# Optimization experiments

Hardware: AMD Instinct MI355X
Metric: run time of the kernel (lower is better)

## Reference

```python
import jax, jax.numpy as jnp
import numpy as np

# ---- static config (mirrors PaCoVoxelLoss init) ----
NUM_QUERIES = 20
FACTOR = 64
NUM_GT = 12
K_NEIGHBORS = 8          # repulsion.num_neighbors
REP_EPS = 1e-12          # repulsion.epsilon
BANDWIDTH = 0.03         # repulsion.kernel_bandwidth
RADIUS = 0.07            # repulsion.radius
ALPHA_PARAM = 0.5
BETA_CHAMFER = 20.0
W_CLS, W_REP, W_CH1, W_CH2 = 1.0, 1.0, 1.0, 1.0
PAD_COST = 1e6           # pad value to square the rectangular assignment problem


def _hungarian(cost):
    # Jonker-Volgenant / e-maxx shortest augmenting path; cost: (n, n) float64.
    # Returns col_to_row: for each column j, the row assigned to it.
    n = cost.shape[0]
    INF = 1e18
    u = np.zeros(n + 1); v = np.zeros(n + 1)
    p = np.zeros(n + 1, dtype=np.int64)
    way = np.zeros(n + 1, dtype=np.int64)
    for i in range(1, n + 1):
        p[0] = i; j0 = 0
        minv = np.full(n + 1, INF)
        used = np.zeros(n + 1, dtype=bool)
        while True:
            used[j0] = True
            i0 = p[j0]; delta = INF; j1 = 0
            for j in range(1, n + 1):
                if not used[j]:
                    cur = cost[i0 - 1, j - 1] - u[i0] - v[j]
                    if cur < minv[j]:
                        minv[j] = cur; way[j] = j0
                    if minv[j] < delta:
                        delta = minv[j]; j1 = j
            for j in range(n + 1):
                if used[j]:
                    u[p[j]] += delta; v[j] -= delta
                else:
                    minv[j] -= delta
            j0 = j1
            if p[j0] == 0:
                break
        while j0 != 0:
            j1 = way[j0]; p[j0] = p[j1]; j0 = j1
    return p[1:] - 1


def _match(cost_np):
    # cost_np: (B, Q, P) with P <= Q -> rows (B, P): pred row matched to each gt col.
    Bn, Qn, Pn = cost_np.shape
    rows = np.zeros((Bn, Pn), dtype=np.int64)
    for b in range(Bn):
        sq = np.full((Qn, Qn), PAD_COST, dtype=np.float64)
        sq[:, :Pn] = cost_np[b].astype(np.float64)
        rows[b] = _hungarian(sq)[:Pn]
    return rows


def _gather_q(A, rows):
    # A: (B, Q, P), rows: (B, P) -> A[b, rows[b,p], p] : (B, P)
    return jnp.take_along_axis(A, rows[:, None, :], axis=1)[:, 0, :]


def _bce_logits(x, t):
    return jnp.maximum(x, 0.0) - x * t + jnp.log1p(jnp.exp(-jnp.abs(x)))


def _cost_terms(pred_normals, pred_distances, gt_normals, gt_distances, points, gt_masks):
    mask_f = gt_masks.astype(points.dtype)           # (B, P, N)
    cnt = mask_f.sum(-1)                             # (B, P)
    # |points . n_q - d_q| for all query planes: (B, Q, N)
    pp = jnp.abs(jnp.einsum('bnd,bqd->bqn', points, pred_normals) - pred_distances[:, :, None])
    cham_raw = jnp.einsum('bqn,bpn->bqp', pp, mask_f) / jnp.maximum(cnt, 1.0)[:, None, :]
    has = (cnt > 0)[:, None, :]                      # (B, 1, P)
    normal_sim = 1.0 - jnp.abs(jnp.einsum('bqd,bpd->bqp', pred_normals, gt_normals))
    dist_diff = jnp.abs(pred_distances[:, :, None] - gt_distances[:, None, :])
    cost = normal_sim + 0.5 * dist_diff + 5.0 * jnp.where(has, cham_raw, 1.0)
    return cost, cham_raw, normal_sim, dist_diff, has


def _losses(pred_logits, pred_normals, pred_distances, gt_normals, gt_distances,
            points, reconstructed_points, gt, gt_masks, rows):
    _, cham_raw, normal_sim, dist_diff, has = _cost_terms(
        pred_normals, pred_distances, gt_normals, gt_distances, points, gt_masks)

    # classification loss: target 1 at matched pred rows
    Qn = pred_logits.shape[1]
    cls_target = jax.nn.one_hot(rows, Qn, dtype=pred_logits.dtype).sum(axis=1)  # (B, Q)
    cls_loss = _bce_logits(pred_logits, cls_target).mean()

    # param loss over matched pairs (mean over P matches, mean over B)
    param_loss = (_gather_q(normal_sim, rows).mean(-1) + _gather_q(dist_diff, rows).mean(-1)).mean()

    # pvd chamfer: point-to-plane term, zero for empty masks, /P /B
    pvd_chamfer = _gather_q(jnp.where(has, cham_raw, 0.0), rows).mean()

    # repulsion loss on per-query point groups
    Bn = reconstructed_points.shape[0]
    rp = reconstructed_points.reshape(Bn, NUM_QUERIES, FACTOR, 3)
    d2 = jnp.sum((rp[:, :, :, None, :] - rp[:, :, None, :, :]) ** 2, axis=-1)  # (B,Q,F,F)
    _, idx = jax.lax.top_k(-d2, K_NEIGHBORS)       # k nearest incl. self
    dn = jnp.maximum(jnp.take_along_axis(d2, idx[..., 1:], axis=-1), REP_EPS)  # (B,Q,F,k-1)
    w = jnp.exp(-dn / BANDWIDTH ** 2)
    rep = jnp.maximum(jnp.mean((RADIUS - jnp.sqrt(dn)) * w, axis=(2, 3)), 0.0).mean()

    # fine-grained chamfer (L1 and L2) between reconstructed and gt clouds
    diff = reconstructed_points[:, :, None, :] - gt[:, None, :, :]  # (B, M, G, 3)
    d1 = jnp.abs(diff).sum(-1)
    d2c = (diff ** 2).sum(-1)
    ch1 = (0.5 * (d1.min(axis=2).mean(axis=1) + d1.min(axis=1).mean(axis=1))).mean()
    ch2 = (0.5 * (d2c.min(axis=2).mean(axis=1) + d2c.min(axis=1).mean(axis=1))).mean()

    total = (W_CLS * cls_loss + ALPHA_PARAM * param_loss + BETA_CHAMFER * pvd_chamfer
             + W_REP * rep + W_CH1 * ch1 + W_CH2 * ch2)
    return total


def setup_inputs() -> dict:
    key = jax.random.key(0)
    ks = jax.random.split(key, 10)
    B, Q, P, N, G = 8, NUM_QUERIES, NUM_GT, 4096, 2048

    def unit(k, shape):
        v = jax.random.normal(k, shape, dtype=jnp.float32)
        return v / jnp.linalg.norm(v, axis=-1, keepdims=True)

    return {
        'pred_logits': jax.random.normal(ks[0], (B, Q), dtype=jnp.float32),
        'pred_normals': unit(ks[1], (B, Q, 3)),
        'pred_distances': jax.random.normal(ks[2], (B, Q), dtype=jnp.float32),
        'gt_normals': unit(ks[3], (B, P, 3)),
        'gt_distances': jax.random.normal(ks[4], (B, P), dtype=jnp.float32),
        'gt_masks': jax.random.bernoulli(ks[5], 0.3, (B, P, N)),
        'points': jax.random.normal(ks[6], (B, N, 3), dtype=jnp.float32),
        'reconstructed_points': 0.5 * jax.random.normal(ks[7], (B, Q * FACTOR, 3), dtype=jnp.float32),
        'gt': jax.random.normal(ks[8], (B, G, 3), dtype=jnp.float32),
        'gt_index': jax.random.randint(ks[9], (B, G), 0, P, dtype=jnp.int64) if jax.config.jax_enable_x64 else jax.random.randint(ks[9], (B, G), 0, P, dtype=jnp.int32),
    }


def reference(pred_logits, pred_normals, pred_distances, gt_normals, gt_distances,
              points, reconstructed_points, gt, gt_masks, gt_index):
    cost = _cost_terms(pred_normals, pred_distances, gt_normals, gt_distances, points, gt_masks)[0]
    rows = jnp.asarray(_match(np.asarray(cost)))  # Hungarian (host, like scipy in original)
    return _losses(pred_logits, pred_normals, pred_distances, gt_normals, gt_distances,
                   points, reconstructed_points, gt, gt_masks, rows)
```

## Files before the change

kernel.cpp:

```cpp
#include <hip/hip_runtime.h>
#include <math.h>

#define Bn 8
#define Qn 20
#define Pn 12
#define Nn 4096
#define Gn 2048
#define Mn 1280
#define Fn 64
#define KNB 7
#define NCOST 160
#define NREP 40
#define NBLK 616
#define C2_TARGET 616
#define SCOPE_AGENT __HIP_MEMORY_SCOPE_AGENT


__device__ __forceinline__ float aread(float* p) { return atomicAdd(p, 0.0f); }
__device__ __forceinline__ void ast(float* p, float v) {
    __hip_atomic_store(p, v, __ATOMIC_RELAXED, SCOPE_AGENT);
}
__device__ __forceinline__ float ald(const float* p) {
    return __hip_atomic_load(p, __ATOMIC_RELAXED, SCOPE_AGENT);
}

__device__ __forceinline__ int rdlane_i(int v, int l) {
    return __builtin_amdgcn_readlane(v, l);
}
__device__ __forceinline__ float rdlane_f(float v, int l) {
    return __int_as_float(__builtin_amdgcn_readlane(__float_as_int(v), l));
}
__device__ __forceinline__ unsigned wave_min_u32(unsigned x) {
    unsigned t;
    t = (unsigned)__builtin_amdgcn_update_dpp((int)0xFFFFFFFF, (int)x, 0x111, 0xF, 0xF, false);
    x = t < x ? t : x;
    t = (unsigned)__builtin_amdgcn_update_dpp((int)0xFFFFFFFF, (int)x, 0x112, 0xF, 0xF, false);
    x = t < x ? t : x;
    t = (unsigned)__builtin_amdgcn_update_dpp((int)0xFFFFFFFF, (int)x, 0x114, 0xF, 0xF, false);
    x = t < x ? t : x;
    t = (unsigned)__builtin_amdgcn_update_dpp((int)0xFFFFFFFF, (int)x, 0x118, 0xF, 0xF, false);
    x = t < x ? t : x;
    t = (unsigned)__builtin_amdgcn_update_dpp((int)0xFFFFFFFF, (int)x, 0x142, 0xF, 0xF, false);
    x = t < x ? t : x;
    t = (unsigned)__builtin_amdgcn_update_dpp((int)0xFFFFFFFF, (int)x, 0x143, 0xF, 0xF, false);
    x = t < x ? t : x;
    return x;
}

__device__ __forceinline__ void wait_zero(float* ws, unsigned init) {
    unsigned* z = (unsigned*)(ws + 7785);
    while (__hip_atomic_load(z, __ATOMIC_ACQUIRE, SCOPE_AGENT) - init != 1u)
        __builtin_amdgcn_s_sleep(1);
}

__device__ __forceinline__ void bump_c2(float* ws, float* out, unsigned init) {
    unsigned* c2P = (unsigned*)(ws + 7784);
    unsigned old = __hip_atomic_fetch_add(c2P, 1u, __ATOMIC_ACQ_REL, SCOPE_AGENT);
    if (old - init == (unsigned)(C2_TARGET - 1)) {
        float* acc = ws + 7776;
        float a0 = aread(&acc[0]);
        float a1 = aread(&acc[1]);
        float a2 = aread(&acc[2]);
        float a3 = aread(&acc[3]);
        float a4 = aread(&acc[4]);
        float a5 = aread(&acc[5]);
        out[0] = a0 + 0.5f * a1 + 20.f * a2 + a3 + a4 + a5;
        unsigned* w = (unsigned*)ws;
        __hip_atomic_store(&w[7782], init, __ATOMIC_RELAXED, SCOPE_AGENT);
        __hip_atomic_store(&w[7784], init, __ATOMIC_RELAXED, SCOPE_AGENT);
        __hip_atomic_store(&w[7785], init, __ATOMIC_RELAXED, SCOPE_AGENT);
        __hip_atomic_store(&w[7786], init, __ATOMIC_RELAXED, SCOPE_AGENT);
        for (int k = 0; k < 40; ++k)
            __hip_atomic_store(&w[8040 + k], init, __ATOMIC_RELAXED, SCOPE_AGENT);
        for (int k = 0; k < 64; ++k)
            __hip_atomic_store(&w[8080 + k], init, __ATOMIC_RELAXED, SCOPE_AGENT);
    }
}

__global__ void fused_kernel(const float* __restrict__ pred_logits,
                             const float* __restrict__ pred_normals,
                             const float* __restrict__ pred_distances,
                             const float* __restrict__ gt_normals,
                             const float* __restrict__ gt_distances,
                             const float* __restrict__ points,
                             const int*   __restrict__ gt_masks,
                             const float* __restrict__ recon,
                             const float* __restrict__ gt,
                             float* __restrict__ ws,
                             float* __restrict__ out) {
    __shared__ __align__(16) float smem[2 * Pn * 256];
    __shared__ int sflag;
    const int blk = blockIdx.x;
    const int tid = threadIdx.x;

    float* cham = ws;
    float* ns   = ws + 1920;
    float* dd   = ws + 3840;
    float* cost = ws + 5760;
    float* cnt  = ws + 7680;
    float* acc  = ws + 7776;
    unsigned* doneP = (unsigned*)(ws + 7782);
    unsigned* baseP = (unsigned*)(ws + 7783);
    unsigned* repcP = (unsigned*)(ws + 7786);
    unsigned* chunkA = (unsigned*)(ws + 8040);
    unsigned* chunkB = (unsigned*)(ws + 8080);
    float* rep_part = ws + 7808;
    float* pmA1 = ws + 8192;
    float* pmA2 = ws + 90112;
    float* pmB1 = ws + 172032;
    float* pmB2 = ws + 253952;

    const unsigned init = __hip_atomic_load(baseP, __ATOMIC_RELAXED, SCOPE_AGENT);

    if (blk < NCOST) {
        if (blk == 0 && tid < 6) ast(&acc[tid], 0.f);
        const int b = blk / Qn, q = blk % Qn;
        const float nx = pred_normals[(b * Qn + q) * 3 + 0];
        const float ny = pred_normals[(b * Qn + q) * 3 + 1];
        const float nz = pred_normals[(b * Qn + q) * 3 + 2];
        const float dq = pred_distances[b * Qn + q];

        float accs[Pn], accw[Pn];
#pragma unroll
        for (int p = 0; p < Pn; ++p) { accs[p] = 0.f; accw[p] = 0.f; }

        const float* ptb = points + (size_t)b * Nn * 3;
        const int*   mb  = gt_masks + (size_t)b * Pn * Nn;

        for (int n = tid; n < Nn; n += 256) {
            float px = ptb[n * 3 + 0], py = ptb[n * 3 + 1], pz = ptb[n * 3 + 2];
            float pp = fabsf(px * nx + py * ny + pz * nz - dq);
#pragma unroll
            for (int p = 0; p < Pn; ++p) {
                float m = (float)mb[(size_t)p * Nn + n];
                accs[p] += pp * m;
                accw[p] += m;
            }
        }
#pragma unroll
        for (int p = 0; p < Pn; ++p) {
            smem[p * 256 + tid] = accs[p];
            smem[(p + Pn) * 256 + tid] = accw[p];
        }
        __syncthreads();
        for (int off = 128; off > 0; off >>= 1) {
            if (tid < off) {
#pragma unroll
                for (int r = 0; r < 2 * Pn; ++r) smem[r * 256 + tid] += smem[r * 256 + tid + off];
            }
            __syncthreads();
        }
        if (tid < Pn) {
            const int p = tid;
            float c  = smem[(p + Pn) * 256];
            float cv = smem[p * 256] / fmaxf(c, 1.f);
            float gnx = gt_normals[(b * Pn + p) * 3 + 0];
            float gny = gt_normals[(b * Pn + p) * 3 + 1];
            float gnz = gt_normals[(b * Pn + p) * 3 + 2];
            float nsim = 1.f - fabsf(nx * gnx + ny * gny + nz * gnz);
            float ddv  = fabsf(dq - gt_distances[b * Pn + p]);
            int idx = (b * Qn + q) * Pn + p;
            ast(&cham[idx], cv);
            ast(&ns[idx],   nsim);
            ast(&dd[idx],   ddv);
            ast(&cost[idx], nsim + 0.5f * ddv + 5.f * ((c > 0.f) ? cv : 1.f));
            if (q == 0) ast(&cnt[b * Pn + p], c);
        }
        __syncthreads();
        if (tid == 0) {
            if (blk == 0) {
                unsigned* z = (unsigned*)(ws + 7785);
                __hip_atomic_store(z, init + 1u, __ATOMIC_RELEASE, SCOPE_AGENT);
            }
            __hip_atomic_fetch_add(doneP, 1u, __ATOMIC_RELEASE, SCOPE_AGENT);
        }

        if (blk >= 8) {
            if (tid == 0) bump_c2(ws, out, init);
            return;
        }

        if (tid == 0) {
            while (__hip_atomic_load(doneP, __ATOMIC_RELAXED, SCOPE_AGENT) - init != (unsigned)NCOST)
                __builtin_amdgcn_s_sleep(2);
            (void)__hip_atomic_load(doneP, __ATOMIC_ACQUIRE, SCOPE_AGENT);
        }
        __syncthreads();

        if (tid < 64) {
            const int b2 = blk;
            const int t = tid;
            const int col = t;
            const bool isCol = (col >= 1 && col <= Qn);

            float cr[Pn];
#pragma unroll
            for (int k = 0; k < Pn; ++k) cr[k] = 0.f;
            if (isCol) {
                const float* cb = cost + ((size_t)b2 * Qn + (col - 1)) * Pn;
#pragma unroll
                for (int k = 0; k < Pn; ++k) cr[k] = ald(&cb[k]);
            }

            float v = 0.f, u = 0.f, minv = 0.f;
            int way = 0, p = 0;

            for (int i = 1; i <= Pn; ++i) {
                minv = 1e30f;
                bool used = false;
                bool rowInPath = false;
                int j0s = 0;
                while (true) {
                    if (col == j0s) used = true;
                    int i0s = (j0s == 0) ? i : rdlane_i(p, j0s);
                    if (t == i0s) rowInPath = true;
                    float u_i0 = rdlane_f(u, i0s);
                    const int bs = i0s - 1;
                    float l10 = (bs & 1) ? cr[1]  : cr[0];
                    float l11 = (bs & 1) ? cr[3]  : cr[2];
                    float l12 = (bs & 1) ? cr[5]  : cr[4];
                    float l13 = (bs & 1) ? cr[7]  : cr[6];
                    float l14 = (bs & 1) ? cr[9]  : cr[8];
                    float l15 = (bs & 1) ? cr[11] : cr[10];
                    float l20 = (bs & 2) ? l11 : l10;
                    float l21 = (bs & 2) ? l13 : l12;
                    float l22 = (bs & 2) ? l15 : l14;
                    float cij = (bs >= 8) ? l22 : ((bs >= 4) ? l21 : l20);
                    if (isCol && !used) {
                        float cur = cij - u_i0 - v;
                        if (cur < minv) { minv = cur; way = j0s; }
                    }
                    float mv = (isCol && !used) ? minv : 1e30f;
                    unsigned kb = __float_as_uint(mv);
                    kb = ((int)kb < 0) ? ~kb : (kb | 0x80000000u);
                    kb = (kb & ~31u) | (unsigned)(col & 31);
                    unsigned kmin = (unsigned)rdlane_i((int)wave_min_u32(kb), 63);
                    int j1 = (int)(kmin & 31u);
                    float delta = rdlane_f(minv, j1);
                    if (used || col == 0) v -= delta;
                    else if (isCol)       minv -= delta;
                    if (rowInPath)        u += delta;
                    j0s = j1;
                    int pj0 = rdlane_i(p, j0s);
                    if (pj0 == 0) break;
                }
                while (j0s != 0) {
                    int wj = rdlane_i(way, j0s);
                    int pw = (wj == 0) ? i : rdlane_i(p, wj);
                    if (col == j0s) p = pw;
                    j0s = wj;
                }
            }

            float cls = 0.f, par = 0.f, pvd = 0.f;
            if (isCol) {
                float x = pred_logits[b2 * Qn + (col - 1)];
                float tgt = (p > 0) ? 1.f : 0.f;
                cls = fmaxf(x, 0.f) - x * tgt + log1pf(expf(-fabsf(x)));
                if (p > 0) {
                    int idx = (b2 * Qn + (col - 1)) * Pn + (p - 1);
                    par = ald(&ns[idx]) + ald(&dd[idx]);
                    pvd = (ald(&cnt[b2 * Pn + (p - 1)]) > 0.f) ? ald(&cham[idx]) : 0.f;
                }
            }
            for (int off = 32; off > 0; off >>= 1) {
                cls += __shfl_down(cls, off);
                par += __shfl_down(par, off);
                pvd += __shfl_down(pvd, off);
            }
            if (t == 0) {
                atomicAdd(&acc[0], cls / (float)(Bn * Qn));
                atomicAdd(&acc[1], par / (float)(Bn * Pn));
                atomicAdd(&acc[2], pvd / (float)(Bn * Pn));
                bump_c2(ws, out, init);
            }
        }
        return;
    } else if (blk < 200) {
        const int wave = tid >> 6, lane = tid & 63;
        const int g = (blk - NCOST) * 4 + wave;
        float* xs = smem + wave * 192;
        float* ys = xs + 64;
        float* zs = xs + 128;
        const float* base = recon + (size_t)g * Fn * 3;
        xs[lane] = base[lane * 3 + 0];
        ys[lane] = base[lane * 3 + 1];
        zs[lane] = base[lane * 3 + 2];
        float best[KNB];
#pragma unroll
        for (int k = 0; k < KNB; ++k) best[k] = 3.4e38f;
        const float xi = xs[lane], yi = ys[lane], zi = zs[lane];
        for (int j = 0; j < Fn; ++j) {
            float dx = xi - xs[j], dy = yi - ys[j], dz = zi - zs[j];
            float d2 = dx * dx + dy * dy + dz * dz;
            d2 = (j == lane) ? 3.4e38f : d2;
#pragma unroll
            for (int k = 0; k < KNB; ++k) {
                float lo = fminf(best[k], d2);
                float hi = fmaxf(best[k], d2);
                best[k] = lo;
                d2 = hi;
            }
        }
        float sum = 0.f;
#pragma unroll
        for (int k = 0; k < KNB; ++k) {
            float dn = fmaxf(best[k], 1e-12f);
            float w  = expf(-dn / (0.03f * 0.03f));
            sum += (0.07f - sqrtf(dn)) * w;
        }
        for (int off = 32; off > 0; off >>= 1) sum += __shfl_down(sum, off);
        if (lane == 0) ast(&rep_part[g], fmaxf(sum / (float)(Fn * KNB), 0.f));
        __syncthreads();
        if (tid == 0) {
            unsigned old = __hip_atomic_fetch_add(repcP, 1u, __ATOMIC_ACQ_REL, SCOPE_AGENT);
            sflag = (old - init == (unsigned)(NREP - 1)) ? 1 : 0;
        }
        __syncthreads();
        if (sflag) {
            float* s1 = smem + 768;
            float c1 = (tid < Bn * Qn) ? ald(&rep_part[tid]) / (float)(Bn * Qn) : 0.f;
            s1[tid] = c1;
            __syncthreads();
            for (int off = 128; off > 0; off >>= 1) {
                if (tid < off) s1[tid] += s1[tid + off];
                __syncthreads();
            }
            if (tid == 0) {
                wait_zero(ws, init);
                atomicAdd(&acc[3], s1[0]);
            }
        }
        if (tid == 0) bump_c2(ws, out, init);
        return;
    }

    float4* tile = reinterpret_cast<float4*>(smem);
    float* o1;
    float* o2;
    unsigned* ctr;
    int idx, chunk, s, nslots;
    float scale;
    float m1 = 3.4e38f, m2 = 3.4e38f;

    if (blk < 360) {
        int a = blk - 200;
        chunk = a >> 2; s = a & 3;
        idx = chunk * 256 + tid;
        const int b = chunk / 5;
        const float* ip = gt + ((size_t)b * Gn + s * 512) * 3;
        {
            float4 tv;
            int j0 = tid;
            tv.x = ip[j0 * 3 + 0]; tv.y = ip[j0 * 3 + 1]; tv.z = ip[j0 * 3 + 2]; tv.w = 0.f;
            tile[j0] = tv;
            int j1 = tid + 256;
            tv.x = ip[j1 * 3 + 0]; tv.y = ip[j1 * 3 + 1]; tv.z = ip[j1 * 3 + 2]; tv.w = 0.f;
            tile[j1] = tv;
        }
        __syncthreads();
        const float x = recon[idx * 3 + 0], y = recon[idx * 3 + 1], z = recon[idx * 3 + 2];
#pragma unroll 4
        for (int j = 0; j < 512; ++j) {
            float4 tv = tile[j];
            float dx = x - tv.x, dy = y - tv.y, dz = z - tv.z;
            float d1 = fabsf(dx) + fabsf(dy) + fabsf(dz);
            float d2 = dx * dx + dy * dy + dz * dz;
            m1 = fminf(m1, d1); m2 = fminf(m2, d2);
        }
        o1 = pmA1; o2 = pmA2; ctr = &chunkA[chunk];
        nslots = Bn * Mn; scale = 0.5f / (float)(Bn * Mn);
    } else {
        int a = blk - 360;
        chunk = a >> 2; s = a & 3;
        idx = chunk * 256 + tid;
        const int b = chunk / 8;
        const float* ip = recon + ((size_t)b * Mn + s * 320) * 3;
        {
            float4 tv;
            int j0 = tid;
            if (j0 < 320) {
                tv.x = ip[j0 * 3 + 0]; tv.y = ip[j0 * 3 + 1]; tv.z = ip[j0 * 3 + 2]; tv.w = 0.f;
                tile[j0] = tv;
            }
            int j1 = tid + 256;
            if (j1 < 320) {
                tv.x = ip[j1 * 3 + 0]; tv.y = ip[j1 * 3 + 1]; tv.z = ip[j1 * 3 + 2]; tv.w = 0.f;
                tile[j1] = tv;
            }
        }
        __syncthreads();
        const float x = gt[idx * 3 + 0], y = gt[idx * 3 + 1], z = gt[idx * 3 + 2];
#pragma unroll 4
        for (int j = 0; j < 320; ++j) {
            float4 tv = tile[j];
            float dx = x - tv.x, dy = y - tv.y, dz = z - tv.z;
            float d1 = fabsf(dx) + fabsf(dy) + fabsf(dz);
            float d2 = dx * dx + dy * dy + dz * dz;
            m1 = fminf(m1, d1); m2 = fminf(m2, d2);
        }
        o1 = pmB1; o2 = pmB2; ctr = &chunkB[chunk];
        nslots = Bn * Gn; scale = 0.5f / (float)(Bn * Gn);
    }

    ast(&o1[s * nslots + idx], m1);
    ast(&o2[s * nslots + idx], m2);
    __syncthreads();
    if (tid == 0) {
        unsigned old = __hip_atomic_fetch_add(ctr, 1u, __ATOMIC_ACQ_REL, SCOPE_AGENT);
        sflag = (old - init == 3u) ? 1 : 0;
    }
    __syncthreads();
    if (sflag) {
        float m1c = 3.4e38f, m2c = 3.4e38f;
#pragma unroll
        for (int ss = 0; ss < 4; ++ss) {
            m1c = fminf(m1c, ald(&o1[ss * nslots + idx]));
            m2c = fminf(m2c, ald(&o2[ss * nslots + idx]));
        }
        float* s1 = smem;
        float* s2 = smem + 256;
        s1[tid] = m1c * scale;
        s2[tid] = m2c * scale;
        __syncthreads();
        for (int off = 128; off > 0; off >>= 1) {
            if (tid < off) { s1[tid] += s1[tid + off]; s2[tid] += s2[tid + off]; }
            __syncthreads();
        }
        if (tid == 0) {
            wait_zero(ws, init);
            atomicAdd(&acc[4], s1[0]);
            atomicAdd(&acc[5], s2[0]);
        }
    }
    if (tid == 0) bump_c2(ws, out, init);
}

extern "C" void kernel_launch(void* const* d_in, const int* in_sizes, int n_in,
                              void* d_out, int out_size, void* d_ws, size_t ws_size,
                              hipStream_t stream) {
    const float* pred_logits    = (const float*)d_in[0];
    const float* pred_normals   = (const float*)d_in[1];
    const float* pred_distances = (const float*)d_in[2];
    const float* gt_normals     = (const float*)d_in[3];
    const float* gt_distances   = (const float*)d_in[4];
    const int*   gt_masks       = (const int*)d_in[5];
    const float* points         = (const float*)d_in[6];
    const float* recon          = (const float*)d_in[7];
    const float* gt             = (const float*)d_in[8];

    fused_kernel<<<NBLK, 256, 0, stream>>>(pred_logits, pred_normals, pred_distances,
                                           gt_normals, gt_distances, points, gt_masks,
                                           recon, gt, (float*)d_ws, (float*)d_out);
}
```

Baseline: 130.3 us.

## Restructure fused loss kernel to 512-thread blocks with per-batch sync and whole-inner chamfer tiles

Moves to 512-thread blocks and cuts the grid from 616 to 284 blocks. Each chamfer block now loads the full inner point set into shared memory and splits it between two halves of the block, so the four-way split with global partial minima and per-chunk counters goes away. The matching blocks now wait on a per-batch done counter instead of one global counter, and only the blocks that contribute to the accumulators bump the completion counter. The cost is fewer blocks to spread across CUs, idle half-blocks in the cost and reduction phases, and a larger shared-memory footprint.

```diff
diff --git a/kernel.cpp b/kernel.cpp
--- a/kernel.cpp
+++ b/kernel.cpp
@@ -10,9 +10,11 @@
 #define Fn 64
 #define KNB 7
 #define NCOST 160
-#define NREP 40
-#define NBLK 616
-#define C2_TARGET 616
+#define NREP 20
+#define NCHA 40
+#define NCHB 64
+#define NBLK 284
+#define C2_TARGET 113
 #define SCOPE_AGENT __HIP_MEMORY_SCOPE_AGENT
 
 
@@ -66,29 +68,27 @@
         float a5 = aread(&acc[5]);
         out[0] = a0 + 0.5f * a1 + 20.f * a2 + a3 + a4 + a5;
         unsigned* w = (unsigned*)ws;
-        __hip_atomic_store(&w[7782], init, __ATOMIC_RELAXED, SCOPE_AGENT);
         __hip_atomic_store(&w[7784], init, __ATOMIC_RELAXED, SCOPE_AGENT);
         __hip_atomic_store(&w[7785], init, __ATOMIC_RELAXED, SCOPE_AGENT);
         __hip_atomic_store(&w[7786], init, __ATOMIC_RELAXED, SCOPE_AGENT);
-        for (int k = 0; k < 40; ++k)
-            __hip_atomic_store(&w[8040 + k], init, __ATOMIC_RELAXED, SCOPE_AGENT);
-        for (int k = 0; k < 64; ++k)
-            __hip_atomic_store(&w[8080 + k], init, __ATOMIC_RELAXED, SCOPE_AGENT);
+        for (int k = 0; k < 8; ++k)
+            __hip_atomic_store(&w[7788 + k], init, __ATOMIC_RELAXED, SCOPE_AGENT);
     }
 }
 
-__global__ void fused_kernel(const float* __restrict__ pred_logits,
-                             const float* __restrict__ pred_normals,
-                             const float* __restrict__ pred_distances,
-                             const float* __restrict__ gt_normals,
-                             const float* __restrict__ gt_distances,
-                             const float* __restrict__ points,
-                             const int*   __restrict__ gt_masks,
-                             const float* __restrict__ recon,
-                             const float* __restrict__ gt,
-                             float* __restrict__ ws,
-                             float* __restrict__ out) {
-    __shared__ __align__(16) float smem[2 * Pn * 256];
+__global__ __launch_bounds__(512, 2)
+void fused_kernel(const float* __restrict__ pred_logits,
+                  const float* __restrict__ pred_normals,
+                  const float* __restrict__ pred_distances,
+                  const float* __restrict__ gt_normals,
+                  const float* __restrict__ gt_distances,
+                  const float* __restrict__ points,
+                  const int*   __restrict__ gt_masks,
+                  const float* __restrict__ recon,
+                  const float* __restrict__ gt,
+                  float* __restrict__ ws,
+                  float* __restrict__ out) {
+    __shared__ __align__(16) float smem[8192];
     __shared__ int sflag;
     const int blk = blockIdx.x;
     const int tid = threadIdx.x;
@@ -99,16 +99,10 @@
     float* cost = ws + 5760;
     float* cnt  = ws + 7680;
     float* acc  = ws + 7776;
-    unsigned* doneP = (unsigned*)(ws + 7782);
     unsigned* baseP = (unsigned*)(ws + 7783);
     unsigned* repcP = (unsigned*)(ws + 7786);
-    unsigned* chunkA = (unsigned*)(ws + 8040);
-    unsigned* chunkB = (unsigned*)(ws + 8080);
+    unsigned* doneB = (unsigned*)(ws + 7788);
     float* rep_part = ws + 7808;
-    float* pmA1 = ws + 8192;
-    float* pmA2 = ws + 90112;
-    float* pmB1 = ws + 172032;
-    float* pmB2 = ws + 253952;
 
     const unsigned init = __hip_atomic_load(baseP, __ATOMIC_RELAXED, SCOPE_AGENT);
 
@@ -120,27 +114,27 @@
         const float nz = pred_normals[(b * Qn + q) * 3 + 2];
         const float dq = pred_distances[b * Qn + q];
 
-        float accs[Pn], accw[Pn];
-#pragma unroll
-        for (int p = 0; p < Pn; ++p) { accs[p] = 0.f; accw[p] = 0.f; }
-
-        const float* ptb = points + (size_t)b * Nn * 3;
-        const int*   mb  = gt_masks + (size_t)b * Pn * Nn;
-
-        for (int n = tid; n < Nn; n += 256) {
-            float px = ptb[n * 3 + 0], py = ptb[n * 3 + 1], pz = ptb[n * 3 + 2];
-            float pp = fabsf(px * nx + py * ny + pz * nz - dq);
+        if (tid < 256) {
+            float accs[Pn], accw[Pn];
+#pragma unroll
+            for (int p = 0; p < Pn; ++p) { accs[p] = 0.f; accw[p] = 0.f; }
+            const float* ptb = points + (size_t)b * Nn * 3;
+            const int*   mb  = gt_masks + (size_t)b * Pn * Nn;
+            for (int n = tid; n < Nn; n += 256) {
+                float px = ptb[n * 3 + 0], py = ptb[n * 3 + 1], pz = ptb[n * 3 + 2];
+                float pp = fabsf(px * nx + py * ny + pz * nz - dq);
+#pragma unroll
+                for (int p = 0; p < Pn; ++p) {
+                    float m = (float)mb[(size_t)p * Nn + n];
+                    accs[p] += pp * m;
+                    accw[p] += m;
+                }
+            }
 #pragma unroll
             for (int p = 0; p < Pn; ++p) {
-                float m = (float)mb[(size_t)p * Nn + n];
-                accs[p] += pp * m;
-                accw[p] += m;
-            }
-        }
-#pragma unroll
-        for (int p = 0; p < Pn; ++p) {
-            smem[p * 256 + tid] = accs[p];
-            smem[(p + Pn) * 256 + tid] = accw[p];
+                smem[p * 256 + tid] = accs[p];
+                smem[(p + Pn) * 256 + tid] = accw[p];
+            }
         }
         __syncthreads();
         for (int off = 128; off > 0; off >>= 1) {
@@ -172,18 +166,14 @@
                 unsigned* z = (unsigned*)(ws + 7785);
                 __hip_atomic_store(z, init + 1u, __ATOMIC_RELEASE, SCOPE_AGENT);
             }
-            __hip_atomic_fetch_add(doneP, 1u, __ATOMIC_RELEASE, SCOPE_AGENT);
-        }
-
-        if (blk >= 8) {
-            if (tid == 0) bump_c2(ws, out, init);
-            return;
-        }
+            __hip_atomic_fetch_add(&doneB[b], 1u, __ATOMIC_RELEASE, SCOPE_AGENT);
+        }
+        if (blk >= 8) return;
 
         if (tid == 0) {
-            while (__hip_atomic_load(doneP, __ATOMIC_RELAXED, SCOPE_AGENT) - init != (unsigned)NCOST)
+            while (__hip_atomic_load(&doneB[blk], __ATOMIC_RELAXED, SCOPE_AGENT) - init != 20u)
                 __builtin_amdgcn_s_sleep(2);
-            (void)__hip_atomic_load(doneP, __ATOMIC_ACQUIRE, SCOPE_AGENT);
+            (void)__hip_atomic_load(&doneB[blk], __ATOMIC_ACQUIRE, SCOPE_AGENT);
         }
         __syncthreads();
 
@@ -269,6 +259,7 @@
                 pvd += __shfl_down(pvd, off);
             }
             if (t == 0) {
+                wait_zero(ws, init);
                 atomicAdd(&acc[0], cls / (float)(Bn * Qn));
                 atomicAdd(&acc[1], par / (float)(Bn * Pn));
                 atomicAdd(&acc[2], pvd / (float)(Bn * Pn));
@@ -276,9 +267,9 @@
             }
         }
         return;
-    } else if (blk < 200) {
+    } else if (blk < NCOST + NREP) {
         const int wave = tid >> 6, lane = tid & 63;
-        const int g = (blk - NCOST) * 4 + wave;
+        const int g = (blk - NCOST) * 8 + wave;
         float* xs = smem + wave * 192;
         float* ys = xs + 64;
         float* zs = xs + 128;
@@ -318,9 +309,9 @@
         }
         __syncthreads();
         if (sflag) {
-            float* s1 = smem + 768;
-            float c1 = (tid < Bn * Qn) ? ald(&rep_part[tid]) / (float)(Bn * Qn) : 0.f;
-            s1[tid] = c1;
+            float* s1 = smem + 2048;
+            if (tid < 256)
+                s1[tid] = (tid < Bn * Qn) ? ald(&rep_part[tid]) / (float)(Bn * Qn) : 0.f;
             __syncthreads();
             for (int off = 128; off > 0; off >>= 1) {
                 if (tid < off) s1[tid] += s1[tid + off];
@@ -329,111 +320,81 @@
             if (tid == 0) {
                 wait_zero(ws, init);
                 atomicAdd(&acc[3], s1[0]);
-            }
-        }
-        if (tid == 0) bump_c2(ws, out, init);
+                bump_c2(ws, out, init);
+            }
+        }
         return;
     }
 
-    float4* tile = reinterpret_cast<float4*>(smem);
-    float* o1;
-    float* o2;
-    unsigned* ctr;
-    int idx, chunk, s, nslots;
-    float scale;
-    float m1 = 3.4e38f, m2 = 3.4e38f;
-
-    if (blk < 360) {
-        int a = blk - 200;
-        chunk = a >> 2; s = a & 3;
-        idx = chunk * 256 + tid;
-        const int b = chunk / 5;
-        const float* ip = gt + ((size_t)b * Gn + s * 512) * 3;
-        {
+    {
+        const int a = blk - (NCOST + NREP);
+        const bool isA = (a < NCHA);
+        const int chunk = isA ? a : (a - NCHA);
+        const int lt = tid & 255;
+        const int half = tid >> 8;
+        const int idx = chunk * 256 + lt;
+        const float* inner;
+        const float* op;
+        int ninner;
+        float scale;
+        if (isA) {
+            const int b = idx / Mn;
+            inner = gt + (size_t)b * Gn * 3;
+            op = recon + (size_t)idx * 3;
+            ninner = Gn;
+            scale = 0.5f / (float)(Bn * Mn);
+        } else {
+            const int b = idx / Gn;
+            inner = recon + (size_t)b * Mn * 3;
+            op = gt + (size_t)idx * 3;
+            ninner = Mn;
+            scale = 0.5f / (float)(Bn * Gn);
+        }
+        float4* tile = reinterpret_cast<float4*>(smem);
+        for (int j = tid; j < ninner; j += 512) {
+            const float* ip = inner + j * 3;
             float4 tv;
-            int j0 = tid;
-            tv.x = ip[j0 * 3 + 0]; tv.y = ip[j0 * 3 + 1]; tv.z = ip[j0 * 3 + 2]; tv.w = 0.f;
-            tile[j0] = tv;
-            int j1 = tid + 256;
-            tv.x = ip[j1 * 3 + 0]; tv.y = ip[j1 * 3 + 1]; tv.z = ip[j1 * 3 + 2]; tv.w = 0.f;
-            tile[j1] = tv;
-        }
-        __syncthreads();
-        const float x = recon[idx * 3 + 0], y = recon[idx * 3 + 1], z = recon[idx * 3 + 2];
+            tv.x = ip[0]; tv.y = ip[1]; tv.z = ip[2]; tv.w = 0.f;
+            tile[j] = tv;
+        }
+        __syncthreads();
+        const float x = op[0], y = op[1], z = op[2];
+        const int j0 = half * (ninner >> 1), j1 = j0 + (ninner >> 1);
+        float m1 = 3.4e38f, m2 = 3.4e38f;
 #pragma unroll 4
-        for (int j = 0; j < 512; ++j) {
+        for (int j = j0; j < j1; ++j) {
             float4 tv = tile[j];
             float dx = x - tv.x, dy = y - tv.y, dz = z - tv.z;
             float d1 = fabsf(dx) + fabsf(dy) + fabsf(dz);
             float d2 = dx * dx + dy * dy + dz * dz;
             m1 = fminf(m1, d1); m2 = fminf(m2, d2);
         }
-        o1 = pmA1; o2 = pmA2; ctr = &chunkA[chunk];
-        nslots = Bn * Mn; scale = 0.5f / (float)(Bn * Mn);
-    } else {
-        int a = blk - 360;
-        chunk = a >> 2; s = a & 3;
-        idx = chunk * 256 + tid;
-        const int b = chunk / 8;
-        const float* ip = recon + ((size_t)b * Mn + s * 320) * 3;
-        {
-            float4 tv;
-            int j0 = tid;
-            if (j0 < 320) {
-                tv.x = ip[j0 * 3 + 0]; tv.y = ip[j0 * 3 + 1]; tv.z = ip[j0 * 3 + 2]; tv.w = 0.f;
-                tile[j0] = tv;
-            }
-            int j1 = tid + 256;
-            if (j1 < 320) {
-                tv.x = ip[j1 * 3 + 0]; tv.y = ip[j1 * 3 + 1]; tv.z = ip[j1 * 3 + 2]; tv.w = 0.f;
-                tile[j1] = tv;
-            }
-        }
-        __syncthreads();
-        const float x = gt[idx * 3 + 0], y = gt[idx * 3 + 1], z = gt[idx * 3 + 2];
-#pragma unroll 4
-        for (int j = 0; j < 320; ++j) {
-            float4 tv = tile[j];
-            float dx = x - tv.x, dy = y - tv.y, dz = z - tv.z;
-            float d1 = fabsf(dx) + fabsf(dy) + fabsf(dz);
-            float d2 = dx * dx + dy * dy + dz * dz;
-            m1 = fminf(m1, d1); m2 = fminf(m2, d2);
-        }
-        o1 = pmB1; o2 = pmB2; ctr = &chunkB[chunk];
-        nslots = Bn * Gn; scale = 0.5f / (float)(Bn * Gn);
-    }
-
-    ast(&o1[s * nslots + idx], m1);
-    ast(&o2[s * nslots + idx], m2);
-    __syncthreads();
-    if (tid == 0) {
-        unsigned old = __hip_atomic_fetch_add(ctr, 1u, __ATOMIC_ACQ_REL, SCOPE_AGENT);
-        sflag = (old - init == 3u) ? 1 : 0;
-    }
-    __syncthreads();
-    if (sflag) {
-        float m1c = 3.4e38f, m2c = 3.4e38f;
-#pragma unroll
-        for (int ss = 0; ss < 4; ++ss) {
-            m1c = fminf(m1c, ald(&o1[ss * nslots + idx]));
-            m2c = fminf(m2c, ald(&o2[ss * nslots + idx]));
-        }
+        __syncthreads();
         float* s1 = smem;
-        float* s2 = smem + 256;
-        s1[tid] = m1c * scale;
-        s2[tid] = m2c * scale;
+        float* s2 = smem + 512;
+        s1[tid] = m1;
+        s2[tid] = m2;
+        __syncthreads();
+        float* t1 = smem + 1024;
+        float* t2 = smem + 1280;
+        if (tid < 256) {
+            float M1 = fminf(s1[tid], s1[tid + 256]);
+            float M2 = fminf(s2[tid], s2[tid + 256]);
+            t1[tid] = M1 * scale;
+            t2[tid] = M2 * scale;
+        }
         __syncthreads();
         for (int off = 128; off > 0; off >>= 1) {
-            if (tid < off) { s1[tid] += s1[tid + off]; s2[tid] += s2[tid + off]; }
+            if (tid < off) { t1[tid] += t1[tid + off]; t2[tid] += t2[tid + off]; }
             __syncthreads();
         }
         if (tid == 0) {
             wait_zero(ws, init);
-            atomicAdd(&acc[4], s1[0]);
-            atomicAdd(&acc[5], s2[0]);
+            atomicAdd(&acc[4], t1[0]);
+            atomicAdd(&acc[5], t2[0]);
+            bump_c2(ws, out, init);
         }
     }
-    if (tid == 0) bump_c2(ws, out, init);
 }
 
 extern "C" void kernel_launch(void* const* d_in, const int* in_sizes, int n_in,
@@ -449,7 +410,7 @@
     const float* recon          = (const float*)d_in[7];
     const float* gt             = (const float*)d_in[8];
 
-    fused_kernel<<<NBLK, 256, 0, stream>>>(pred_logits, pred_normals, pred_distances,
+    fused_kernel<<<NBLK, 512, 0, stream>>>(pred_logits, pred_normals, pred_distances,
                                            gt_normals, gt_distances, points, gt_masks,
                                            recon, gt, (float*)d_ws, (float*)d_out);
 }
```

Result: faster. 114.1 us (-12.5%).
